# Optimization experiments

Measured on AMD Instinct MI355X. Metric: run time of the kernel, lower is better.

Reference implementation:

```python
import jax, jax.numpy as jnp
import numpy as np

BSZ, NLVL, E, H, FFN = 8, 4, 512, 8, 2048
D = E // H
NNZ = 131072
LMAX = NNZ // BSZ  # equal per-batch counts -> static padded length
THETA = 10.0


def _layernorm(x, g, b):
    mu = x.mean(-1, keepdims=True)
    var = ((x - mu) ** 2).mean(-1, keepdims=True)
    return (x - mu) / jnp.sqrt(var + 1e-5) * g + b


def _rope(x, pos, freqs):
    # x: [N, E], pos: [N] float, freqs: [H, D/2] -> rotate interleaved pairs per head
    N = x.shape[0]
    nh, half = freqs.shape
    xr = x.reshape(N, nh, half, 2)
    ang = pos[:, None, None] * freqs[None]            # [N, H, D/2]
    c, s = jnp.cos(ang), jnp.sin(ang)
    x1, x2 = xr[..., 0], xr[..., 1]
    out = jnp.stack([x1 * c - x2 * s, x1 * s + x2 * c], axis=-1)
    return out.reshape(N, -1)


def setup_inputs() -> dict:
    key = jax.random.key(0)
    ks = jax.random.split(key, 8)
    bg = jax.random.normal(ks[0], (BSZ, NLVL, E), jnp.float32)
    feature_values = jax.random.normal(ks[1], (NNZ, E), jnp.float32)
    # coalesced sparse COO -> batch indices sorted; equal counts per batch for static shapes
    feature_batch_idx = (jnp.arange(NNZ, dtype=jnp.int32) // LMAX)
    feature_level_idx = jax.random.randint(ks[2], (NNZ,), 0, NLVL, dtype=jnp.int32)
    s = 1.0 / np.sqrt(E)
    Wq = jax.random.normal(ks[3], (E, E), jnp.float32) * s
    Wkv = jax.random.normal(ks[4], (E, 2 * E), jnp.float32) * s
    Wo = jax.random.normal(ks[5], (E, E), jnp.float32) * s
    freqs = THETA ** (-jnp.arange(D // 2, dtype=jnp.float32) * 2.0 / D)
    rope_freqs = jnp.tile(freqs[None, :], (H, 1))  # share_heads=False: per-head table
    ln_attn_g, ln_attn_b = jnp.ones(E, jnp.float32), jnp.zeros(E, jnp.float32)
    ln_ffn_g, ln_ffn_b = jnp.ones(E, jnp.float32), jnp.zeros(E, jnp.float32)
    W1 = jax.random.normal(ks[6], (E, FFN), jnp.float32) * s
    b1 = jnp.zeros(FFN, jnp.float32)
    W2 = jax.random.normal(ks[7], (FFN, E), jnp.float32) * (1.0 / np.sqrt(FFN))
    b2 = jnp.zeros(E, jnp.float32)
    return {
        'bg': bg, 'feature_values': feature_values,
        'feature_batch_idx': feature_batch_idx, 'feature_level_idx': feature_level_idx,
        'Wq': Wq, 'Wkv': Wkv, 'Wo': Wo, 'rope_freqs': rope_freqs,
        'ln_attn_g': ln_attn_g, 'ln_attn_b': ln_attn_b,
        'ln_ffn_g': ln_ffn_g, 'ln_ffn_b': ln_ffn_b,
        'W1': W1, 'b1': b1, 'W2': W2, 'b2': b2,
        'max_len': LMAX,
    }


def reference(bg, feature_values, feature_batch_idx, feature_level_idx,
              Wq, Wkv, Wo, rope_freqs, ln_attn_g, ln_attn_b,
              ln_ffn_g, ln_ffn_b, W1, b1, W2, b2, max_len):
    bsz, nlvl, e = bg.shape
    nh = rope_freqs.shape[0]
    d = e // nh
    nnz = feature_values.shape[0]

    # --- attention block (pre-norm) ---
    residual = bg
    x = _layernorm(bg, ln_attn_g, ln_attn_b)
    q = (x @ Wq).reshape(bsz * nlvl, e)
    kv = feature_values @ Wkv
    k, v = kv[:, :e], kv[:, e:]

    # RoPE on level indices (replicates original's repeat_interleave ordering: level = i // bsz)
    q_lvl = (jnp.arange(bsz * nlvl) // bsz).astype(jnp.float32)
    q = _rope(q, q_lvl, rope_freqs)
    k = _rope(k, feature_level_idx.astype(jnp.float32), rope_freqs)

    # concatenated (ragged) -> padded per batch
    counts = jax.ops.segment_sum(jnp.ones(nnz, jnp.int32), feature_batch_idx, num_segments=bsz)
    offsets = jnp.concatenate([jnp.zeros(1, jnp.int32), jnp.cumsum(counts)[:-1].astype(jnp.int32)])
    pos = jnp.arange(nnz, dtype=jnp.int32) - offsets[feature_batch_idx]
    k_pad = jnp.zeros((bsz, max_len, e), k.dtype).at[feature_batch_idx, pos].set(k)
    v_pad = jnp.zeros((bsz, max_len, e), v.dtype).at[feature_batch_idx, pos].set(v)
    pad_mask = jnp.arange(max_len)[None, :] >= counts[:, None]  # True at padding

    # SDPA
    qh = q.reshape(bsz, nlvl, nh, d).transpose(0, 2, 1, 3)
    kh = k_pad.reshape(bsz, max_len, nh, d).transpose(0, 2, 1, 3)
    vh = v_pad.reshape(bsz, max_len, nh, d).transpose(0, 2, 1, 3)
    scores = jnp.einsum('bhqd,bhkd->bhqk', qh, kh) / jnp.sqrt(jnp.asarray(d, qh.dtype))
    scores = jnp.where(pad_mask[:, None, None, :], -jnp.inf, scores)
    attn = jax.nn.softmax(scores, axis=-1)
    o = jnp.einsum('bhqk,bhkd->bhqd', attn, vh).transpose(0, 2, 1, 3).reshape(bsz, nlvl, e)
    o = o @ Wo + residual

    # --- FFN block (pre-norm) ---
    y = _layernorm(o, ln_ffn_g, ln_ffn_b)
    y = jax.nn.relu(y @ W1 + b1) @ W2 + b2
    return o + y
```

## Files before the change

### kernel.cpp

```cpp
#include <hip/hip_runtime.h>
#include <hip/hip_bf16.h>
#include <math.h>

#define BSZ 8
#define NLVL 4
#define E 512
#define H 8
#define D 64
#define FFN 2048
#define NNZ 131072
#define NQ 32
#define P32 32
#define NEGF -3.0e38f

typedef __attribute__((ext_vector_type(8))) short bf16x8;
typedef __attribute__((ext_vector_type(4))) float f32x4;

#define WS_QROT   16
#define WS_WSUM   (WS_QROT + NQ*E)
#define WS_OATT   (WS_WSUM + BSZ*P32*E)
#define WS_O2     (WS_OATT + NQ*E)
#define WS_Y      (WS_O2 + NQ*E)
#define WS_HID    (WS_Y + NQ*E)
#define WS_PART   (WS_HID + NQ*FFN)
#define WS_ML     (WS_PART + 512*P32*E)
#define WS_WALL   (WS_ML + 512*P32*2)

__device__ inline short f2bf(float x) {
    __hip_bfloat16 h = __float2bfloat16(x);
    union { __hip_bfloat16 v; short s; } u; u.v = h; return u.s;
}

__global__ void k_zero(int* wsi) {
    if (blockIdx.x == 0 && threadIdx.x < 8) wsi[threadIdx.x] = 0;
}

__global__ void k_hist(const int* __restrict__ fb, int* wsi) {
    __shared__ int h[8];
    int t = threadIdx.x;
    if (t < 8) h[t] = 0;
    __syncthreads();
    for (int j = blockIdx.x * 256 + t; j < NNZ; j += gridDim.x * 256)
        atomicAdd(&h[fb[j]], 1);
    __syncthreads();
    if (t < 8) atomicAdd(&wsi[t], h[t]);
}

__global__ void k_off(int* wsi) {
    if (threadIdx.x == 0) {
        int run = 0;
        for (int b = 0; b < 8; b++) { wsi[8 + b] = run; run += wsi[b]; }
    }
}

__global__ void k_qrot(const float* __restrict__ bg, const float* __restrict__ Wq,
                       const float* __restrict__ rf, const float* __restrict__ g,
                       const float* __restrict__ bb, float* __restrict__ ws) {
    __shared__ float xr[E];
    __shared__ float qrow[E];
    __shared__ float red[8];
    int r = blockIdx.x, t = threadIdx.x;
    float v0 = bg[r * E + t], v1 = bg[r * E + t + 256];
    float s = v0 + v1;
    for (int o = 32; o > 0; o >>= 1) s += __shfl_down(s, o, 64);
    if ((t & 63) == 0) red[t >> 6] = s;
    __syncthreads();
    if (t == 0) red[0] = (red[0] + red[1] + red[2] + red[3]) * (1.0f / E);
    __syncthreads();
    float mu = red[0];
    __syncthreads();
    float d0 = v0 - mu, d1 = v1 - mu;
    s = d0 * d0 + d1 * d1;
    for (int o = 32; o > 0; o >>= 1) s += __shfl_down(s, o, 64);
    if ((t & 63) == 0) red[t >> 6] = s;
    __syncthreads();
    if (t == 0) red[0] = rsqrtf((red[0] + red[1] + red[2] + red[3]) * (1.0f / E) + 1e-5f);
    __syncthreads();
    float rstd = red[0];
    xr[t] = d0 * rstd * g[t] + bb[t];
    xr[t + 256] = d1 * rstd * g[t + 256] + bb[t + 256];
    __syncthreads();
    for (int half = 0; half < 2; half++) {
        int c = t + half * 256;
        float acc = 0.f;
        for (int e = 0; e < E; e++) acc += xr[e] * Wq[e * E + c];
        qrow[c] = acc;
    }
    __syncthreads();
    int c0 = 2 * t, c1 = c0 + 1;
    int h = c0 >> 6, ii = (c0 & 63) >> 1;
    float freq = rf[h * 32 + ii];
    float pos = (float)(r >> 3);
    float a = pos * freq, ca = cosf(a), sa = sinf(a);
    float x1 = qrow[c0], x2 = qrow[c1];
    float* qr = ws + WS_QROT + r * E;
    qr[c0] = x1 * ca - x2 * sa;
    qr[c1] = x1 * sa + x2 * ca;
}

__global__ void k_wtil(const float* __restrict__ Wkv, const float* __restrict__ rf,
                       const float* __restrict__ ws, short* __restrict__ wall) {
    __shared__ float u[D];
    int blk = blockIdx.x;
    int h = blk & 7, lvl = (blk >> 3) & 3, r = blk >> 5;
    int b = r >> 2, l = r & 3;
    int t = threadIdx.x;
    const float* qr = ws + WS_QROT + r * E + h * D;
    if (t < 32) {
        float freq = rf[h * 32 + t];
        float a = (float)lvl * freq;
        float ca = cosf(a), sa = sinf(a);
        float x1 = qr[2 * t], x2 = qr[2 * t + 1];
        u[2 * t] = x1 * ca + x2 * sa;
        u[2 * t + 1] = -x1 * sa + x2 * ca;
    }
    __syncthreads();
    int n = lvl * 32 + l * 8 + h;
    short* wrow_out = wall + ((size_t)(b * 128 + n)) * E;
    for (int rep = 0; rep < 8; rep++) {
        int e = t + rep * 64;
        const float* wrow = Wkv + (size_t)e * (2 * E) + h * D;
        float acc = 0.f;
#pragma unroll
        for (int c = 0; c < D; c++) acc += wrow[c] * u[c];
        wrow_out[e] = f2bf(acc * 0.125f);
    }
}

#define KSTR 520
#define TSTR 40
__global__ __launch_bounds__(256, 2) void k_flash(
    const float* __restrict__ fv, const int* __restrict__ fl,
    const short* __restrict__ wall, const int* __restrict__ wsi,
    const int* __restrict__ maxlen, float* __restrict__ part, float* __restrict__ ml) {
    __shared__ short kbuf[32 * KSTR];
    __shared__ short fvT[512 * TSTR];
    __shared__ short pbuf[32 * TSTR];
    __shared__ float mbuf[4 * 32];
    __shared__ float lpart[4 * 32];
    __shared__ float alph[32];
    __shared__ float mrun[32];
    __shared__ float lrun[32];

    int t = threadIdx.x;
    int w = t >> 6, lane = t & 63, col = lane & 15, quad = lane >> 4;
    int b = blockIdx.x, kc = blockIdx.y;
    int cnt = wsi[b], mlen = maxlen[0];
    int lim = cnt < mlen ? cnt : mlen;
    int off = wsi[8 + b];
    int kbase = kc * 256;
    int nv = lim - kbase; if (nv > 256) nv = 256; if (nv < 0) nv = 0;

    if (t < 32) { mrun[t] = NEGF; lrun[t] = 0.f; }

    f32x4 acc_o[2][8];
#pragma unroll
    for (int mt = 0; mt < 2; mt++)
#pragma unroll
        for (int nt = 0; nt < 8; nt++) acc_o[mt][nt] = f32x4{0.f, 0.f, 0.f, 0.f};

    const short* wallb = wall + (size_t)b * 128 * E;
    int sj = (t & 15) * 2;
    int se = (t >> 4) * 32;

    for (int s = 0; s < 8; s++) {
        int vs = nv - s * 32;
        if (vs <= 0) break;
        __syncthreads();
        {
            int g0 = off + kbase + s * 32 + sj;
            int g1 = g0 + 1;
            if (g0 > NNZ - 1) g0 = NNZ - 1;
            if (g1 > NNZ - 1) g1 = NNZ - 1;
            const float* r0 = fv + (size_t)g0 * E + se;
            const float* r1 = fv + (size_t)g1 * E + se;
#pragma unroll
            for (int i = 0; i < 8; i++) {
                float4 x0 = *(const float4*)(r0 + i * 4);
                float4 x1 = *(const float4*)(r1 + i * 4);
                int e = se + i * 4;
                *(__hip_bfloat162*)&kbuf[sj * KSTR + e]       = __float22bfloat162_rn(float2{x0.x, x0.y});
                *(__hip_bfloat162*)&kbuf[sj * KSTR + e + 2]   = __float22bfloat162_rn(float2{x0.z, x0.w});
                *(__hip_bfloat162*)&kbuf[(sj+1) * KSTR + e]   = __float22bfloat162_rn(float2{x1.x, x1.y});
                *(__hip_bfloat162*)&kbuf[(sj+1) * KSTR + e+2] = __float22bfloat162_rn(float2{x1.z, x1.w});
                *(__hip_bfloat162*)&fvT[(e + 0) * TSTR + sj] = __float22bfloat162_rn(float2{x0.x, x1.x});
                *(__hip_bfloat162*)&fvT[(e + 1) * TSTR + sj] = __float22bfloat162_rn(float2{x0.y, x1.y});
                *(__hip_bfloat162*)&fvT[(e + 2) * TSTR + sj] = __float22bfloat162_rn(float2{x0.z, x1.z});
                *(__hip_bfloat162*)&fvT[(e + 3) * TSTR + sj] = __float22bfloat162_rn(float2{x0.w, x1.w});
            }
        }
        __syncthreads();
        f32x4 acc_s[2][2];
#pragma unroll
        for (int mt = 0; mt < 2; mt++)
#pragma unroll
            for (int kt = 0; kt < 2; kt++) acc_s[mt][kt] = f32x4{0.f, 0.f, 0.f, 0.f};
        {
            const short* wr0 = wallb + (size_t)(w * 32 + col) * E + quad * 8;
            const short* wr1 = wr0 + (size_t)16 * E;
            const short* kb0 = &kbuf[col * KSTR + quad * 8];
            const short* kb1 = &kbuf[(16 + col) * KSTR + quad * 8];
#pragma unroll
            for (int ks = 0; ks < 16; ks++) {
                int e0 = ks * 32;
                bf16x8 A0 = *(const bf16x8*)(wr0 + e0);
                bf16x8 A1 = *(const bf16x8*)(wr1 + e0);
                bf16x8 B0 = *(const bf16x8*)(kb0 + e0);
                bf16x8 B1 = *(const bf16x8*)(kb1 + e0);
                acc_s[0][0] = __builtin_amdgcn_mfma_f32_16x16x32_bf16(A0, B0, acc_s[0][0], 0, 0, 0);
                acc_s[0][1] = __builtin_amdgcn_mfma_f32_16x16x32_bf16(A0, B1, acc_s[0][1], 0, 0, 0);
                acc_s[1][0] = __builtin_amdgcn_mfma_f32_16x16x32_bf16(A1, B0, acc_s[1][0], 0, 0, 0);
                acc_s[1][1] = __builtin_amdgcn_mfma_f32_16x16x32_bf16(A1, B1, acc_s[1][1], 0, 0, 0);
            }
        }
        int kg0 = off + kbase + s * 32 + col;
        int kg1 = kg0 + 16;
        if (kg0 > NNZ - 1) kg0 = NNZ - 1;
        if (kg1 > NNZ - 1) kg1 = NNZ - 1;
        int lv0 = fl[kg0], lv1 = fl[kg1];
        bool valid0 = (s * 32 + col) < nv;
        bool valid1 = (s * 32 + 16 + col) < nv;
        bool sel0 = valid0 && (lv0 == w);
        bool sel1 = valid1 && (lv1 == w);
#pragma unroll
        for (int mt = 0; mt < 2; mt++) {
#pragma unroll
            for (int r = 0; r < 4; r++) {
                float v0 = sel0 ? acc_s[mt][0][r] : NEGF;
                float v1 = sel1 ? acc_s[mt][1][r] : NEGF;
                float v = fmaxf(v0, v1);
#pragma unroll
                for (int msk = 1; msk < 16; msk <<= 1) v = fmaxf(v, __shfl_xor(v, msk, 16));
                if (col == 0) mbuf[w * 32 + mt * 16 + quad * 4 + r] = v;
            }
        }
        __syncthreads();
        if (t < 32) {
            int p = t;
            float mo = mrun[p];
            float mn = mo;
            mn = fmaxf(mn, mbuf[p]);
            mn = fmaxf(mn, mbuf[32 + p]);
            mn = fmaxf(mn, mbuf[64 + p]);
            mn = fmaxf(mn, mbuf[96 + p]);
            alph[p] = expf(mo - mn);
            mrun[p] = mn;
        }
        __syncthreads();
        float mr[2][4], ar[2][4];
#pragma unroll
        for (int mt = 0; mt < 2; mt++)
#pragma unroll
            for (int r = 0; r < 4; r++) {
                int p = mt * 16 + quad * 4 + r;
                mr[mt][r] = mrun[p];
                ar[mt][r] = alph[p];
            }
#pragma unroll
        for (int mt = 0; mt < 2; mt++) {
#pragma unroll
            for (int r = 0; r < 4; r++) {
                int p = mt * 16 + quad * 4 + r;
                float ls = 0.f;
                {
                    if (sel0) {
                        float pv = expf(acc_s[mt][0][r] - mr[mt][r]);
                        pbuf[p * TSTR + col] = f2bf(pv);
                        ls += pv;
                    } else if (w == 0 && !valid0) {
                        pbuf[p * TSTR + col] = 0;
                    }
                    if (sel1) {
                        float pv = expf(acc_s[mt][1][r] - mr[mt][r]);
                        pbuf[p * TSTR + 16 + col] = f2bf(pv);
                        ls += pv;
                    } else if (w == 0 && !valid1) {
                        pbuf[p * TSTR + 16 + col] = 0;
                    }
                }
#pragma unroll
                for (int msk = 1; msk < 16; msk <<= 1) ls += __shfl_xor(ls, msk, 16);
                if (col == 0) lpart[w * 32 + p] = ls;
            }
        }
#pragma unroll
        for (int mt = 0; mt < 2; mt++)
#pragma unroll
            for (int nt = 0; nt < 8; nt++)
#pragma unroll
                for (int r = 0; r < 4; r++) acc_o[mt][nt][r] *= ar[mt][r];
        __syncthreads();
        {
            bf16x8 Ap0 = *(const bf16x8*)&pbuf[col * TSTR + quad * 8];
            bf16x8 Ap1 = *(const bf16x8*)&pbuf[(16 + col) * TSTR + quad * 8];
            const short* bt = &fvT[(size_t)(w * 128 + col) * TSTR + quad * 8];
#pragma unroll
            for (int nt = 0; nt < 8; nt++) {
                bf16x8 Bf = *(const bf16x8*)(bt + (size_t)nt * 16 * TSTR);
                acc_o[0][nt] = __builtin_amdgcn_mfma_f32_16x16x32_bf16(Ap0, Bf, acc_o[0][nt], 0, 0, 0);
                acc_o[1][nt] = __builtin_amdgcn_mfma_f32_16x16x32_bf16(Ap1, Bf, acc_o[1][nt], 0, 0, 0);
            }
        }
        if (t < 32) {
            int p = t;
            lrun[p] = lrun[p] * alph[p] + (lpart[p] + lpart[32 + p] + lpart[64 + p] + lpart[96 + p]);
        }
    }
    size_t pbase = ((size_t)(b * 64 + kc) * P32) * E;
#pragma unroll
    for (int mt = 0; mt < 2; mt++)
#pragma unroll
        for (int r = 0; r < 4; r++) {
            int p = mt * 16 + quad * 4 + r;
#pragma unroll
            for (int nt = 0; nt < 8; nt++) {
                int e = w * 128 + nt * 16 + col;
                part[pbase + (size_t)p * E + e] = acc_o[mt][nt][r];
            }
        }
    if (t < 32) {
        size_t idx = (size_t)(b * 64 + kc) * P32 + t;
        ml[idx * 2] = mrun[t];
        ml[idx * 2 + 1] = lrun[t];
    }
}

__global__ void k_merge(const float* __restrict__ part, const float* __restrict__ ml,
                        float* __restrict__ wsum) {
    __shared__ float wexp[64];
    int b = blockIdx.x >> 5, p = blockIdx.x & 31;
    int t = threadIdx.x;
    float M = NEGF;
    for (int kc = 0; kc < 64; kc++)
        M = fmaxf(M, ml[((size_t)(b * 64 + kc) * P32 + p) * 2]);
    float denom = 0.f;
    for (int kc = 0; kc < 64; kc++) {
        size_t idx = ((size_t)(b * 64 + kc) * P32 + p) * 2;
        denom += ml[idx + 1] * expf(ml[idx] - M);
    }
    if (t < 64)
        wexp[t] = expf(ml[((size_t)(b * 64 + t) * P32 + p) * 2] - M);
    __syncthreads();
    float inv = 1.0f / denom;
    for (int half = 0; half < 2; half++) {
        int e = t + half * 256;
        float acc = 0.f;
        for (int kc = 0; kc < 64; kc++)
            acc += part[((size_t)(b * 64 + kc) * P32 + p) * E + e] * wexp[kc];
        wsum[((size_t)(b * P32 + p)) * E + e] = acc * inv;
    }
}

__global__ void k_oproj(const float* __restrict__ wsum, const float* __restrict__ Wkv,
                        float* __restrict__ oatt) {
    __shared__ float Aw[NQ][E];
    int h = blockIdx.x >> 2, ct = blockIdx.x & 3;
    int t = threadIdx.x;
    {
        int rr = t >> 3, x = (t & 7) * 64;
        int row = (rr >> 2) * P32 + (rr & 3) * 8 + h;
#pragma unroll
        for (int q4 = 0; q4 < 16; q4++)
            *(float4*)&Aw[rr][x + q4 * 4] = *(const float4*)&wsum[(size_t)row * E + x + q4 * 4];
    }
    __syncthreads();
#pragma unroll
    for (int rep = 0; rep < 2; rep++) {
        int idx = rep * 256 + t;
        int rr = idx >> 4, cl = idx & 15;
        int c = h * D + ct * 16 + cl;
        float acc = 0.f;
        for (int e = 0; e < E; e++) acc += Aw[rr][e] * Wkv[(size_t)e * (2 * E) + E + c];
        oatt[rr * E + c] = acc;
    }
}

__global__ void k_wo(const float* __restrict__ oatt, const float* __restrict__ Wo,
                     const float* __restrict__ bg, float* __restrict__ o2) {
    __shared__ float Aw[NQ * E];
    int t = threadIdx.x;
#pragma unroll
    for (int q = 0; q < 16; q++) {
        int i = (q * 256 + t) * 4;
        *(float4*)&Aw[i] = *(const float4*)&oatt[i];
    }
    __syncthreads();
    int ct = blockIdx.x;
#pragma unroll
    for (int rep = 0; rep < 4; rep++) {
        int idx = rep * 256 + t;
        int rr = idx >> 5, cl = idx & 31;
        int c = ct * 32 + cl;
        float acc = bg[rr * E + c];
        for (int e = 0; e < E; e++) acc += Aw[rr * E + e] * Wo[(size_t)e * E + c];
        o2[rr * E + c] = acc;
    }
}

__global__ void k_ln2(const float* __restrict__ o2, const float* __restrict__ g,
                      const float* __restrict__ bb, float* __restrict__ y) {
    __shared__ float red[8];
    int r = blockIdx.x, t = threadIdx.x;
    float v0 = o2[r * E + t], v1 = o2[r * E + t + 256];
    float s = v0 + v1;
    for (int o = 32; o > 0; o >>= 1) s += __shfl_down(s, o, 64);
    if ((t & 63) == 0) red[t >> 6] = s;
    __syncthreads();
    if (t == 0) red[0] = (red[0] + red[1] + red[2] + red[3]) * (1.0f / E);
    __syncthreads();
    float mu = red[0];
    __syncthreads();
    float d0 = v0 - mu, d1 = v1 - mu;
    s = d0 * d0 + d1 * d1;
    for (int o = 32; o > 0; o >>= 1) s += __shfl_down(s, o, 64);
    if ((t & 63) == 0) red[t >> 6] = s;
    __syncthreads();
    if (t == 0) red[0] = rsqrtf((red[0] + red[1] + red[2] + red[3]) * (1.0f / E) + 1e-5f);
    __syncthreads();
    float rstd = red[0];
    y[r * E + t] = d0 * rstd * g[t] + bb[t];
    y[r * E + t + 256] = d1 * rstd * g[t + 256] + bb[t + 256];
}

__global__ void k_ffn1(const float* __restrict__ y, const float* __restrict__ W1,
                       const float* __restrict__ b1, float* __restrict__ hid) {
    __shared__ float Aw[NQ * E];
    int t = threadIdx.x;
#pragma unroll
    for (int q = 0; q < 16; q++) {
        int i = (q * 256 + t) * 4;
        *(float4*)&Aw[i] = *(const float4*)&y[i];
    }
    __syncthreads();
    int ft = blockIdx.x;
#pragma unroll
    for (int rep = 0; rep < 4; rep++) {
        int idx = rep * 256 + t;
        int rr = idx >> 5, fl = idx & 31;
        int f = ft * 32 + fl;
        float acc = b1[f];
        for (int e = 0; e < E; e++) acc += Aw[rr * E + e] * W1[(size_t)e * FFN + f];
        hid[rr * FFN + f] = fmaxf(acc, 0.f);
    }
}

__global__ void k_ffn2(const float* __restrict__ hid, const float* __restrict__ W2,
                       const float* __restrict__ b2, const float* __restrict__ o2,
                       float* __restrict__ out) {
    int ct = blockIdx.x;
    int t = threadIdx.x;
#pragma unroll
    for (int rep = 0; rep < 2; rep++) {
        int idx = rep * 256 + t;
        int rr = idx >> 4, cl = idx & 15;
        int c = ct * 16 + cl;
        float acc = b2[c] + o2[rr * E + c];
        for (int f = 0; f < FFN; f++) acc += hid[rr * FFN + f] * W2[(size_t)f * E + c];
        out[rr * E + c] = acc;
    }
}

extern "C" void kernel_launch(void* const* d_in, const int* in_sizes, int n_in,
                              void* d_out, int out_size, void* d_ws, size_t ws_size,
                              hipStream_t stream) {
    const float* bg  = (const float*)d_in[0];
    const float* fv  = (const float*)d_in[1];
    const int*   fb  = (const int*)d_in[2];
    const int*   fl  = (const int*)d_in[3];
    const float* Wq  = (const float*)d_in[4];
    const float* Wkv = (const float*)d_in[5];
    const float* Wo  = (const float*)d_in[6];
    const float* rf  = (const float*)d_in[7];
    const float* lag = (const float*)d_in[8];
    const float* lab = (const float*)d_in[9];
    const float* lfg = (const float*)d_in[10];
    const float* lfb = (const float*)d_in[11];
    const float* W1  = (const float*)d_in[12];
    const float* b1  = (const float*)d_in[13];
    const float* W2  = (const float*)d_in[14];
    const float* b2  = (const float*)d_in[15];
    const int* maxlen = (const int*)d_in[16];
    float* ws = (float*)d_ws;
    int* wsi = (int*)d_ws;
    short* wall = (short*)(ws + WS_WALL);
    float* out = (float*)d_out;

    hipLaunchKernelGGL(k_zero, dim3(1), dim3(64), 0, stream, wsi);
    hipLaunchKernelGGL(k_hist, dim3(128), dim3(256), 0, stream, fb, wsi);
    hipLaunchKernelGGL(k_off, dim3(1), dim3(64), 0, stream, wsi);
    hipLaunchKernelGGL(k_qrot, dim3(NQ), dim3(256), 0, stream, bg, Wq, rf, lag, lab, ws);
    hipLaunchKernelGGL(k_wtil, dim3(NQ * NLVL * H), dim3(64), 0, stream, Wkv, rf, ws, wall);
    hipLaunchKernelGGL(k_flash, dim3(BSZ, 64), dim3(256), 0, stream,
                       fv, fl, wall, wsi, maxlen, ws + WS_PART, ws + WS_ML);
    hipLaunchKernelGGL(k_merge, dim3(BSZ * P32), dim3(256), 0, stream,
                       ws + WS_PART, ws + WS_ML, ws + WS_WSUM);
    hipLaunchKernelGGL(k_oproj, dim3(H * 4), dim3(256), 0, stream,
                       ws + WS_WSUM, Wkv, ws + WS_OATT);
    hipLaunchKernelGGL(k_wo, dim3(16), dim3(256), 0, stream,
                       ws + WS_OATT, Wo, bg, ws + WS_O2);
    hipLaunchKernelGGL(k_ln2, dim3(NQ), dim3(256), 0, stream,
                       ws + WS_O2, lfg, lfb, ws + WS_Y);
    hipLaunchKernelGGL(k_ffn1, dim3(FFN / 32), dim3(256), 0, stream,
                       ws + WS_Y, W1, b1, ws + WS_HID);
    hipLaunchKernelGGL(k_ffn2, dim3(E / 16), dim3(256), 0, stream,
                       ws + WS_HID, W2, b2, ws + WS_O2, out);
}
```

Before: 864.2 us.

## Split flash chunks finer, drop K smem buffer, keep softmax stats per-lane

The key chunk per block shrinks from 256 to 128 rows, doubling the grid to 8x128 blocks, and the launch bound rises to 3 blocks per CU. The score MFMA now reads feature rows straight from global memory and converts them to bf16 in registers, so the large kbuf shared buffer goes away. Each wave writes its own slice of the transposed V tile, and the running max and sum live in registers, which removes two of the per-step barriers. In exchange, feature values are read from global memory twice and the merge kernel has twice as many partials to read and reduce.

```diff
diff --git a/kernel.cpp b/kernel.cpp
--- a/kernel.cpp
+++ b/kernel.cpp
@@ -11,6 +11,7 @@
 #define NNZ 131072
 #define NQ 32
 #define P32 32
+#define NCH 128
 #define NEGF -3.0e38f
 
 typedef __attribute__((ext_vector_type(8))) short bf16x8;
@@ -23,12 +24,23 @@
 #define WS_Y      (WS_O2 + NQ*E)
 #define WS_HID    (WS_Y + NQ*E)
 #define WS_PART   (WS_HID + NQ*FFN)
-#define WS_ML     (WS_PART + 512*P32*E)
-#define WS_WALL   (WS_ML + 512*P32*2)
+#define WS_ML     (WS_PART + BSZ*NCH*P32*E)
+#define WS_WALL   (WS_ML + BSZ*NCH*P32*2)
 
 __device__ inline short f2bf(float x) {
     __hip_bfloat16 h = __float2bfloat16(x);
     union { __hip_bfloat16 v; short s; } u; u.v = h; return u.s;
+}
+
+__device__ inline bf16x8 cvt8(const float* p) {
+    float4 x = *(const float4*)p;
+    float4 y = *(const float4*)(p + 4);
+    union { bf16x8 v; __hip_bfloat162 h[4]; } u;
+    u.h[0] = __float22bfloat162_rn(float2{x.x, x.y});
+    u.h[1] = __float22bfloat162_rn(float2{x.z, x.w});
+    u.h[2] = __float22bfloat162_rn(float2{y.x, y.y});
+    u.h[3] = __float22bfloat162_rn(float2{y.z, y.w});
+    return u.v;
 }
 
 __global__ void k_zero(int* wsi) {
@@ -127,20 +139,16 @@
     }
 }
 
-#define KSTR 520
 #define TSTR 40
-__global__ __launch_bounds__(256, 2) void k_flash(
+__global__ __launch_bounds__(256, 3) void k_flash(
     const float* __restrict__ fv, const int* __restrict__ fl,
     const short* __restrict__ wall, const int* __restrict__ wsi,
     const int* __restrict__ maxlen, float* __restrict__ part, float* __restrict__ ml) {
-    __shared__ short kbuf[32 * KSTR];
     __shared__ short fvT[512 * TSTR];
     __shared__ short pbuf[32 * TSTR];
-    __shared__ float mbuf[4 * 32];
-    __shared__ float lpart[4 * 32];
-    __shared__ float alph[32];
-    __shared__ float mrun[32];
-    __shared__ float lrun[32];
+    __shared__ float mbuf[32 * 4];
+    __shared__ float lfin[32 * 4];
+    __shared__ float mfin[32];
 
     int t = threadIdx.x;
     int w = t >> 6, lane = t & 63, col = lane & 15, quad = lane >> 4;
@@ -148,48 +156,45 @@
     int cnt = wsi[b], mlen = maxlen[0];
     int lim = cnt < mlen ? cnt : mlen;
     int off = wsi[8 + b];
-    int kbase = kc * 256;
-    int nv = lim - kbase; if (nv > 256) nv = 256; if (nv < 0) nv = 0;
-
-    if (t < 32) { mrun[t] = NEGF; lrun[t] = 0.f; }
+    int kbase = kc * 128;
+    int nv = lim - kbase; if (nv > 128) nv = 128; if (nv < 0) nv = 0;
 
     f32x4 acc_o[2][8];
 #pragma unroll
     for (int mt = 0; mt < 2; mt++)
 #pragma unroll
         for (int nt = 0; nt < 8; nt++) acc_o[mt][nt] = f32x4{0.f, 0.f, 0.f, 0.f};
+    float mrun[2][4], lrun[2][4];
+#pragma unroll
+    for (int mt = 0; mt < 2; mt++)
+#pragma unroll
+        for (int r = 0; r < 4; r++) { mrun[mt][r] = NEGF; lrun[mt][r] = 0.f; }
 
     const short* wallb = wall + (size_t)b * 128 * E;
-    int sj = (t & 15) * 2;
-    int se = (t >> 4) * 32;
-
-    for (int s = 0; s < 8; s++) {
-        int vs = nv - s * 32;
-        if (vs <= 0) break;
-        __syncthreads();
+    short* fvTw = &fvT[(size_t)w * 128 * TSTR];
+    int k2 = lane & 15;
+    int eseg = lane >> 4;
+
+    for (int s = 0; s < 4; s++) {
+        if (s * 32 >= nv) break;
+        int j0 = off + kbase + s * 32;
         {
-            int g0 = off + kbase + s * 32 + sj;
-            int g1 = g0 + 1;
+            int g0 = j0 + 2 * k2, g1 = g0 + 1;
             if (g0 > NNZ - 1) g0 = NNZ - 1;
             if (g1 > NNZ - 1) g1 = NNZ - 1;
-            const float* r0 = fv + (size_t)g0 * E + se;
-            const float* r1 = fv + (size_t)g1 * E + se;
+            const float* r0 = fv + (size_t)g0 * E + w * 128 + eseg * 32;
+            const float* r1 = fv + (size_t)g1 * E + w * 128 + eseg * 32;
+            short* dst = fvTw + (size_t)(eseg * 32) * TSTR + 2 * k2;
 #pragma unroll
             for (int i = 0; i < 8; i++) {
                 float4 x0 = *(const float4*)(r0 + i * 4);
                 float4 x1 = *(const float4*)(r1 + i * 4);
-                int e = se + i * 4;
-                *(__hip_bfloat162*)&kbuf[sj * KSTR + e]       = __float22bfloat162_rn(float2{x0.x, x0.y});
-                *(__hip_bfloat162*)&kbuf[sj * KSTR + e + 2]   = __float22bfloat162_rn(float2{x0.z, x0.w});
-                *(__hip_bfloat162*)&kbuf[(sj+1) * KSTR + e]   = __float22bfloat162_rn(float2{x1.x, x1.y});
-                *(__hip_bfloat162*)&kbuf[(sj+1) * KSTR + e+2] = __float22bfloat162_rn(float2{x1.z, x1.w});
-                *(__hip_bfloat162*)&fvT[(e + 0) * TSTR + sj] = __float22bfloat162_rn(float2{x0.x, x1.x});
-                *(__hip_bfloat162*)&fvT[(e + 1) * TSTR + sj] = __float22bfloat162_rn(float2{x0.y, x1.y});
-                *(__hip_bfloat162*)&fvT[(e + 2) * TSTR + sj] = __float22bfloat162_rn(float2{x0.z, x1.z});
-                *(__hip_bfloat162*)&fvT[(e + 3) * TSTR + sj] = __float22bfloat162_rn(float2{x0.w, x1.w});
+                *(__hip_bfloat162*)&dst[(i * 4 + 0) * TSTR] = __float22bfloat162_rn(float2{x0.x, x1.x});
+                *(__hip_bfloat162*)&dst[(i * 4 + 1) * TSTR] = __float22bfloat162_rn(float2{x0.y, x1.y});
+                *(__hip_bfloat162*)&dst[(i * 4 + 2) * TSTR] = __float22bfloat162_rn(float2{x0.z, x1.z});
+                *(__hip_bfloat162*)&dst[(i * 4 + 3) * TSTR] = __float22bfloat162_rn(float2{x0.w, x1.w});
             }
         }
-        __syncthreads();
         f32x4 acc_s[2][2];
 #pragma unroll
         for (int mt = 0; mt < 2; mt++)
@@ -198,23 +203,22 @@
         {
             const short* wr0 = wallb + (size_t)(w * 32 + col) * E + quad * 8;
             const short* wr1 = wr0 + (size_t)16 * E;
-            const short* kb0 = &kbuf[col * KSTR + quad * 8];
-            const short* kb1 = &kbuf[(16 + col) * KSTR + quad * 8];
+            const float* fb0 = fv + (size_t)(j0 + col) * E + quad * 8;
+            const float* fb1 = fv + (size_t)(j0 + 16 + col) * E + quad * 8;
 #pragma unroll
             for (int ks = 0; ks < 16; ks++) {
                 int e0 = ks * 32;
                 bf16x8 A0 = *(const bf16x8*)(wr0 + e0);
                 bf16x8 A1 = *(const bf16x8*)(wr1 + e0);
-                bf16x8 B0 = *(const bf16x8*)(kb0 + e0);
-                bf16x8 B1 = *(const bf16x8*)(kb1 + e0);
+                bf16x8 B0 = cvt8(fb0 + e0);
+                bf16x8 B1 = cvt8(fb1 + e0);
                 acc_s[0][0] = __builtin_amdgcn_mfma_f32_16x16x32_bf16(A0, B0, acc_s[0][0], 0, 0, 0);
                 acc_s[0][1] = __builtin_amdgcn_mfma_f32_16x16x32_bf16(A0, B1, acc_s[0][1], 0, 0, 0);
                 acc_s[1][0] = __builtin_amdgcn_mfma_f32_16x16x32_bf16(A1, B0, acc_s[1][0], 0, 0, 0);
                 acc_s[1][1] = __builtin_amdgcn_mfma_f32_16x16x32_bf16(A1, B1, acc_s[1][1], 0, 0, 0);
             }
         }
-        int kg0 = off + kbase + s * 32 + col;
-        int kg1 = kg0 + 16;
+        int kg0 = j0 + col, kg1 = j0 + 16 + col;
         if (kg0 > NNZ - 1) kg0 = NNZ - 1;
         if (kg1 > NNZ - 1) kg1 = NNZ - 1;
         int lv0 = fl[kg0], lv1 = fl[kg1];
@@ -223,7 +227,7 @@
         bool sel0 = valid0 && (lv0 == w);
         bool sel1 = valid1 && (lv1 == w);
 #pragma unroll
-        for (int mt = 0; mt < 2; mt++) {
+        for (int mt = 0; mt < 2; mt++)
 #pragma unroll
             for (int r = 0; r < 4; r++) {
                 float v0 = sel0 ? acc_s[mt][0][r] : NEGF;
@@ -231,82 +235,65 @@
                 float v = fmaxf(v0, v1);
 #pragma unroll
                 for (int msk = 1; msk < 16; msk <<= 1) v = fmaxf(v, __shfl_xor(v, msk, 16));
-                if (col == 0) mbuf[w * 32 + mt * 16 + quad * 4 + r] = v;
-            }
-        }
+                if (col == 0) mbuf[(mt * 16 + quad * 4 + r) * 4 + w] = v;
+            }
         __syncthreads();
-        if (t < 32) {
-            int p = t;
-            float mo = mrun[p];
-            float mn = mo;
-            mn = fmaxf(mn, mbuf[p]);
-            mn = fmaxf(mn, mbuf[32 + p]);
-            mn = fmaxf(mn, mbuf[64 + p]);
-            mn = fmaxf(mn, mbuf[96 + p]);
-            alph[p] = expf(mo - mn);
-            mrun[p] = mn;
-        }
-        __syncthreads();
-        float mr[2][4], ar[2][4];
 #pragma unroll
         for (int mt = 0; mt < 2; mt++)
 #pragma unroll
             for (int r = 0; r < 4; r++) {
                 int p = mt * 16 + quad * 4 + r;
-                mr[mt][r] = mrun[p];
-                ar[mt][r] = alph[p];
-            }
-#pragma unroll
-        for (int mt = 0; mt < 2; mt++) {
-#pragma unroll
-            for (int r = 0; r < 4; r++) {
-                int p = mt * 16 + quad * 4 + r;
-                float ls = 0.f;
-                {
-                    if (sel0) {
-                        float pv = expf(acc_s[mt][0][r] - mr[mt][r]);
-                        pbuf[p * TSTR + col] = f2bf(pv);
-                        ls += pv;
-                    } else if (w == 0 && !valid0) {
-                        pbuf[p * TSTR + col] = 0;
-                    }
-                    if (sel1) {
-                        float pv = expf(acc_s[mt][1][r] - mr[mt][r]);
-                        pbuf[p * TSTR + 16 + col] = f2bf(pv);
-                        ls += pv;
-                    } else if (w == 0 && !valid1) {
-                        pbuf[p * TSTR + 16 + col] = 0;
-                    }
+                f32x4 mm = *(const f32x4*)&mbuf[p * 4];
+                float mn = fmaxf(fmaxf(mm[0], mm[1]), fmaxf(mm[2], mm[3]));
+                mn = fmaxf(mn, mrun[mt][r]);
+                float al = expf(mrun[mt][r] - mn);
+                mrun[mt][r] = mn;
+                float add = 0.f;
+                if (sel0) {
+                    float pv = expf(acc_s[mt][0][r] - mn);
+                    pbuf[p * TSTR + col] = f2bf(pv);
+                    add += pv;
+                } else if (w == 0 && !valid0) {
+                    pbuf[p * TSTR + col] = 0;
                 }
-#pragma unroll
-                for (int msk = 1; msk < 16; msk <<= 1) ls += __shfl_xor(ls, msk, 16);
-                if (col == 0) lpart[w * 32 + p] = ls;
-            }
-        }
-#pragma unroll
-        for (int mt = 0; mt < 2; mt++)
-#pragma unroll
-            for (int nt = 0; nt < 8; nt++)
-#pragma unroll
-                for (int r = 0; r < 4; r++) acc_o[mt][nt][r] *= ar[mt][r];
+                if (sel1) {
+                    float pv = expf(acc_s[mt][1][r] - mn);
+                    pbuf[p * TSTR + 16 + col] = f2bf(pv);
+                    add += pv;
+                } else if (w == 0 && !valid1) {
+                    pbuf[p * TSTR + 16 + col] = 0;
+                }
+                lrun[mt][r] = lrun[mt][r] * al + add;
+#pragma unroll
+                for (int nt = 0; nt < 8; nt++) acc_o[mt][nt][r] *= al;
+            }
         __syncthreads();
         {
             bf16x8 Ap0 = *(const bf16x8*)&pbuf[col * TSTR + quad * 8];
             bf16x8 Ap1 = *(const bf16x8*)&pbuf[(16 + col) * TSTR + quad * 8];
-            const short* bt = &fvT[(size_t)(w * 128 + col) * TSTR + quad * 8];
+            const short* bt = fvTw + (size_t)col * TSTR + quad * 8;
 #pragma unroll
             for (int nt = 0; nt < 8; nt++) {
-                bf16x8 Bf = *(const bf16x8*)(bt + (size_t)nt * 16 * TSTR);
+                bf16x8 Bf = *(const bf16x8*)(bt + (size_t)(nt * 16) * TSTR);
                 acc_o[0][nt] = __builtin_amdgcn_mfma_f32_16x16x32_bf16(Ap0, Bf, acc_o[0][nt], 0, 0, 0);
                 acc_o[1][nt] = __builtin_amdgcn_mfma_f32_16x16x32_bf16(Ap1, Bf, acc_o[1][nt], 0, 0, 0);
             }
         }
-        if (t < 32) {
-            int p = t;
-            lrun[p] = lrun[p] * alph[p] + (lpart[p] + lpart[32 + p] + lpart[64 + p] + lpart[96 + p]);
+    }
+#pragma unroll
+    for (int mt = 0; mt < 2; mt++)
+#pragma unroll
+        for (int r = 0; r < 4; r++) {
+            float ls = lrun[mt][r];
+#pragma unroll
+            for (int msk = 1; msk < 16; msk <<= 1) ls += __shfl_xor(ls, msk, 16);
+            int p = mt * 16 + quad * 4 + r;
+            if (col == 0) {
+                lfin[p * 4 + w] = ls;
+                if (w == 0) mfin[p] = mrun[mt][r];
+            }
         }
-    }
-    size_t pbase = ((size_t)(b * 64 + kc) * P32) * E;
+    size_t pbase = ((size_t)(b * NCH + kc) * P32) * E;
 #pragma unroll
     for (int mt = 0; mt < 2; mt++)
 #pragma unroll
@@ -318,35 +305,37 @@
                 part[pbase + (size_t)p * E + e] = acc_o[mt][nt][r];
             }
         }
+    __syncthreads();
     if (t < 32) {
-        size_t idx = (size_t)(b * 64 + kc) * P32 + t;
-        ml[idx * 2] = mrun[t];
-        ml[idx * 2 + 1] = lrun[t];
+        float l = lfin[t * 4] + lfin[t * 4 + 1] + lfin[t * 4 + 2] + lfin[t * 4 + 3];
+        size_t idx = (size_t)(b * NCH + kc) * P32 + t;
+        ml[idx * 2] = mfin[t];
+        ml[idx * 2 + 1] = l;
     }
 }
 
 __global__ void k_merge(const float* __restrict__ part, const float* __restrict__ ml,
                         float* __restrict__ wsum) {
-    __shared__ float wexp[64];
+    __shared__ float wexp[NCH];
     int b = blockIdx.x >> 5, p = blockIdx.x & 31;
     int t = threadIdx.x;
     float M = NEGF;
-    for (int kc = 0; kc < 64; kc++)
-        M = fmaxf(M, ml[((size_t)(b * 64 + kc) * P32 + p) * 2]);
+    for (int kc = 0; kc < NCH; kc++)
+        M = fmaxf(M, ml[((size_t)(b * NCH + kc) * P32 + p) * 2]);
     float denom = 0.f;
-    for (int kc = 0; kc < 64; kc++) {
-        size_t idx = ((size_t)(b * 64 + kc) * P32 + p) * 2;
+    for (int kc = 0; kc < NCH; kc++) {
+        size_t idx = ((size_t)(b * NCH + kc) * P32 + p) * 2;
         denom += ml[idx + 1] * expf(ml[idx] - M);
     }
-    if (t < 64)
-        wexp[t] = expf(ml[((size_t)(b * 64 + t) * P32 + p) * 2] - M);
+    if (t < NCH)
+        wexp[t] = expf(ml[((size_t)(b * NCH + t) * P32 + p) * 2] - M);
     __syncthreads();
     float inv = 1.0f / denom;
     for (int half = 0; half < 2; half++) {
         int e = t + half * 256;
         float acc = 0.f;
-        for (int kc = 0; kc < 64; kc++)
-            acc += part[((size_t)(b * 64 + kc) * P32 + p) * E + e] * wexp[kc];
+        for (int kc = 0; kc < NCH; kc++)
+            acc += part[((size_t)(b * NCH + kc) * P32 + p) * E + e] * wexp[kc];
         wsum[((size_t)(b * P32 + p)) * E + e] = acc * inv;
     }
 }
@@ -490,7 +479,7 @@
     hipLaunchKernelGGL(k_off, dim3(1), dim3(64), 0, stream, wsi);
     hipLaunchKernelGGL(k_qrot, dim3(NQ), dim3(256), 0, stream, bg, Wq, rf, lag, lab, ws);
     hipLaunchKernelGGL(k_wtil, dim3(NQ * NLVL * H), dim3(64), 0, stream, Wkv, rf, ws, wall);
-    hipLaunchKernelGGL(k_flash, dim3(BSZ, 64), dim3(256), 0, stream,
+    hipLaunchKernelGGL(k_flash, dim3(BSZ, NCH), dim3(256), 0, stream,
                        fv, fl, wall, wsi, maxlen, ws + WS_PART, ws + WS_ML);
     hipLaunchKernelGGL(k_merge, dim3(BSZ * P32), dim3(256), 0, stream,
                        ws + WS_PART, ws + WS_ML, ws + WS_WSUM);
```

Measured after the change: 1.089 ms. 1.26x slower.
